# Performance work log

Hardware: AMD Instinct MI355X
Metric: run time of the kernel (lower is better)

The kernel has to match this reference:

```python
import jax, jax.numpy as jnp
import numpy as np

B, T, D, M = 32, 2048, 128, 256   # batch, seq_len, pitch vocab d, encoder_output_dim m
FILTERS = [256, 256, 256]
TAU = 1.0                          # gumbel_temperature
ALPHA_INV = 1.0 / (D * 100)        # W init value: 1/alpha, alpha = d*100


def causal_dilated_conv(x, w, b, dilation):
    """x: [B,T,Cin], w: [K,Cin,Cout], causal left padding."""
    k = w.shape[0]
    pad = (k - 1) * dilation
    y = jax.lax.conv_general_dilated(
        x, w, window_strides=(1,), padding=[(pad, 0)],
        rhs_dilation=(dilation,),
        dimension_numbers=('NWC', 'WIO', 'NWC'))
    return y + b


def slow_weight_model(batch, w0, b0, w1, b1, w2, b2, w_out, b_out):
    """DilatedConvBlock: stack of causal dilated convs (relu) + 1x1 readout to m logits."""
    h = jax.nn.relu(causal_dilated_conv(batch, w0, b0, dilation=1))
    h = jax.nn.relu(causal_dilated_conv(h, w1, b1, dilation=2))
    h = jax.nn.relu(causal_dilated_conv(h, w2, b2, dilation=4))
    return causal_dilated_conv(h, w_out, b_out, dilation=1)  # [B,T,M] logits


def setup_inputs() -> dict:
    key = jax.random.key(0)
    ks = jax.random.split(key, 9)
    def glorot(k, shape):
        fan_in = np.prod(shape[:-1])
        return (jax.random.normal(k, shape, jnp.float32) / np.sqrt(fan_in)).astype(jnp.float32)
    return {
        'batch': jax.random.uniform(ks[0], (B, T, D), jnp.float32),
        'w0': glorot(ks[1], (2, D, FILTERS[0])), 'b0': jnp.zeros((FILTERS[0],), jnp.float32),
        'w1': glorot(ks[2], (2, FILTERS[0], FILTERS[1])), 'b1': jnp.zeros((FILTERS[1],), jnp.float32),
        'w2': glorot(ks[3], (2, FILTERS[1], FILTERS[2])), 'b2': jnp.zeros((FILTERS[2],), jnp.float32),
        'w_out': glorot(ks[4], (1, FILTERS[2], M)), 'b_out': jnp.zeros((M,), jnp.float32),
    }


def reference(batch, w0, b0, w1, b1, w2, b2, w_out, b_out):
    logits = slow_weight_model(batch, w0, b0, w1, b1, w2, b2, w_out, b_out)  # [B,T,M]
    # short_term_method == 'softmax_normalize_after'
    h_src = jax.nn.softmax(logits / TAU, axis=2)  # [B,T,M]
    s_tar = batch                                  # [B,T,D]
    W0 = jnp.full((B, M, D), ALPHA_INV, jnp.float32)

    def step(W, hs):
        h, s = hs                                              # [B,M], [B,D]
        num = jnp.einsum('bm,bmd->bd', h, W)                   # readout
        prob = num / jnp.sum(num, axis=-1, keepdims=True)      # normalize-after
        W_new = W + h[:, :, None] * s[:, None, :]              # outer-product fast-weight update
        return W_new, prob

    W_final, probs = jax.lax.scan(
        step, W0, (jnp.swapaxes(h_src, 0, 1), jnp.swapaxes(s_tar, 0, 1)))
    probs = jnp.swapaxes(probs, 0, 1)  # [B,T,D]
    return probs, W_final
```

## Files before the change

### kernel.cpp

```cpp
#include <hip/hip_runtime.h>

using u16 = unsigned short;
using u32 = unsigned int;
using short8 = __attribute__((ext_vector_type(8))) short;
using short4v = __attribute__((ext_vector_type(4))) short;
using bf16x8 = __attribute__((ext_vector_type(8))) __bf16;
using f32x4 = __attribute__((ext_vector_type(4))) float;

#define ALPHA_INV (1.0f / (128.0f * 100.0f))

__device__ __forceinline__ u32 swz(u32 off, u32 row) { return off ^ ((row & 7u) << 4); }

__device__ __forceinline__ u16 f2bf(float x) {
  u32 u = __float_as_uint(x);
  u32 r = u + 0x7fffu + ((u >> 16) & 1u);
  return (u16)(r >> 16);
}

__device__ __forceinline__ float bf2f(u16 x) {
  u32 u = ((u32)x) << 16;
  return __uint_as_float(u);
}

__device__ __forceinline__ f32x4 mfma(bf16x8 a, bf16x8 b, f32x4 c) {
  return __builtin_amdgcn_mfma_f32_16x16x32_bf16(a, b, c, 0, 0, 0);
}

__device__ __forceinline__ void gl16(const void* g, void* l) {
  __builtin_amdgcn_global_load_lds(
      (const __attribute__((address_space(1))) unsigned int*)g,
      (__attribute__((address_space(3))) unsigned int*)l, 16, 0, 0);
}

__global__ __launch_bounds__(256) void prep(
    const float* __restrict__ batch,
    const float* __restrict__ w0, const float* __restrict__ w1,
    const float* __restrict__ w2, const float* __restrict__ wo,
    u16* __restrict__ o0, u16* __restrict__ o1,
    u16* __restrict__ o2, u16* __restrict__ o3,
    u16* __restrict__ ST) {
  __shared__ u16 L[64 * 129];
  int blk = blockIdx.x;
  if (blk < 1536) {
    const float* w; u16* o; int cin;
    if (blk < 256)       { w = w0; o = o0; cin = 128; }
    else if (blk < 768)  { w = w1; o = o1; cin = 256; blk -= 256; }
    else if (blk < 1280) { w = w2; o = o2; cin = 256; blk -= 768; }
    else                 { w = wo; o = o3; cin = 256; blk -= 1280; }
    int idx = blk * 256 + threadIdx.x;
    int row = idx >> 8, n = idx & 255;
    int tap = row / cin, c = row - tap * cin;
    int kc = c >> 6, ci = c & 63;
    u32 sb = (u32)(ci * 2) ^ ((u32)(n & 7) << 4);
    o[((size_t)tap * 256 + n) * cin + kc * 64 + (sb >> 1)] = f2bf(w[idx]);
    return;
  }
  blk -= 1536;
  const int tid = threadIdx.x;
  const int t0 = (blk & 31) * 64;
  const int b = blk >> 5;
  const float* src = batch + ((size_t)b * 2048 + t0) * 128;
#pragma unroll
  for (int it = 0; it < 4; ++it) {
    int s = tid + it * 256;
    int t = s >> 4, c8 = s & 15;
    float4 v0 = *(const float4*)(src + t * 128 + c8 * 8);
    float4 v1 = *(const float4*)(src + t * 128 + c8 * 8 + 4);
    u16* p = &L[t * 129 + c8 * 8];
    p[0] = f2bf(v0.x); p[1] = f2bf(v0.y); p[2] = f2bf(v0.z); p[3] = f2bf(v0.w);
    p[4] = f2bf(v1.x); p[5] = f2bf(v1.y); p[6] = f2bf(v1.z); p[7] = f2bf(v1.w);
  }
  __syncthreads();
  u16* dst = ST + (size_t)b * 128 * 2048 + t0;
#pragma unroll
  for (int it = 0; it < 4; ++it) {
    int s = tid + it * 256;
    int oct = s & 7, d = s >> 3;
    short8 v;
#pragma unroll
    for (int j = 0; j < 8; ++j) v[j] = (short)L[(oct * 8 + j) * 129 + d];
    *(short8*)(dst + (size_t)d * 2048 + oct * 8) = v;
  }
}

__global__ __launch_bounds__(512) void conv_first(
    const float* __restrict__ in, const u16* __restrict__ wt,
    const float* __restrict__ bias, u16* __restrict__ out) {
  constexpr int CIN = 128, BN = 256;
  __shared__ alignas(16) u16 Al[128 * 64];
  __shared__ alignas(16) u16 Bl[256 * 64];

  const int tid = threadIdx.x;
  const int wid = tid >> 6, lane = tid & 63;
  const int wr = wid >> 2, wc = wid & 3;
  const int lg = lane >> 4, lq = lane & 15;
  const int row0 = blockIdx.x * 128;
  const int tloc0 = row0 & 2047;

  f32x4 acc[4][4];
#pragma unroll
  for (int i = 0; i < 4; ++i)
#pragma unroll
    for (int j = 0; j < 4; ++j) acc[i][j] = (f32x4)0.0f;

#pragma unroll
  for (int tap = 0; tap < 2; ++tap) {
    const int shift = 1 - tap;
#pragma unroll
    for (int kc = 0; kc < 2; ++kc) {
#pragma unroll
      for (int it = 0; it < 2; ++it) {
        int gi = tid + it * 512;
        int r = gi >> 3, cg = gi & 7;
        short8 v = (short8)0;
        if (!(tloc0 == 0 && r < shift)) {
          const float* src = in + (size_t)(row0 + r - shift) * CIN + kc * 64 + cg * 8;
          float4 a = *(const float4*)src;
          float4 b2 = *(const float4*)(src + 4);
          v[0] = (short)f2bf(a.x);  v[1] = (short)f2bf(a.y);
          v[2] = (short)f2bf(a.z);  v[3] = (short)f2bf(a.w);
          v[4] = (short)f2bf(b2.x); v[5] = (short)f2bf(b2.y);
          v[6] = (short)f2bf(b2.z); v[7] = (short)f2bf(b2.w);
        }
        *(short8*)((char*)Al + swz(r * 128 + cg * 16, (u32)(r - shift + 8))) = v;
      }
      {
        const u16* wtb = wt + ((size_t)(tap * 256)) * CIN + kc * 64;
#pragma unroll
        for (int it = 0; it < 4; ++it) {
          int gi = tid + it * 512;
          int n = gi >> 3, cg = gi & 7;
          gl16(wtb + (size_t)n * CIN + cg * 8, (char*)Bl + it * 8192 + wid * 1024);
        }
      }
      __syncthreads();
#pragma unroll
      for (int ks = 0; ks < 2; ++ks) {
        bf16x8 af[4], bfr[4];
#pragma unroll
        for (int mi = 0; mi < 4; ++mi) {
          int r = wr * 64 + mi * 16 + lq;
          af[mi] = *(const bf16x8*)((const char*)Al +
                                    swz(r * 128 + ks * 64 + lg * 16, (u32)(r - shift + 8)));
        }
#pragma unroll
        for (int ni = 0; ni < 4; ++ni) {
          int n = wc * 64 + ni * 16 + lq;
          bfr[ni] = *(const bf16x8*)((const char*)Bl + swz(n * 128 + ks * 64 + lg * 16, n));
        }
#pragma unroll
        for (int mi = 0; mi < 4; ++mi)
#pragma unroll
          for (int ni = 0; ni < 4; ++ni)
            acc[mi][ni] = mfma(af[mi], bfr[ni], acc[mi][ni]);
      }
      __syncthreads();
    }
  }

  float bcol[4];
#pragma unroll
  for (int ni = 0; ni < 4; ++ni) bcol[ni] = bias[wc * 64 + ni * 16 + lq];
#pragma unroll
  for (int mi = 0; mi < 4; ++mi)
#pragma unroll
    for (int ni = 0; ni < 4; ++ni)
#pragma unroll
      for (int rr = 0; rr < 4; ++rr) {
        float v = fmaxf(acc[mi][ni][rr] + bcol[ni], 0.0f);
        int row = row0 + wr * 64 + mi * 16 + lg * 4 + rr;
        int col = wc * 64 + ni * 16 + lq;
        int ci = col & 63;
        u32 sb = (u32)(ci * 2) ^ ((u32)(row & 7) << 4);
        out[(size_t)row * BN + wc * 64 + (sb >> 1)] = f2bf(v);
      }
}

template <int DIL>
__global__ __launch_bounds__(512) void conv_mid(
    const u16* __restrict__ in, const u16* __restrict__ wt,
    const float* __restrict__ bias, u16* __restrict__ out) {
  constexpr int CIN = 256, BN = 256;
  __shared__ alignas(16) u16 Al[136 * 64];
  __shared__ alignas(16) u16 Bl[256 * 64];

  const int tid = threadIdx.x;
  const int wid = tid >> 6, lane = tid & 63;
  const int wr = wid >> 2, wc = wid & 3;
  const int lg = lane >> 4, lq = lane & 15;
  const int row0 = blockIdx.x * 128;
  const int tloc0 = row0 & 2047;

  f32x4 acc[4][4];
#pragma unroll
  for (int i = 0; i < 4; ++i)
#pragma unroll
    for (int j = 0; j < 4; ++j) acc[i][j] = (f32x4)0.0f;

#pragma unroll
  for (int kc = 0; kc < 4; ++kc) {
#pragma unroll
    for (int p = 0; p < 2; ++p) {
      int gi = tid + p * 512;
      int r = gi >> 3, cg = gi & 7;
      gl16(in + (size_t)(row0 - DIL + r) * CIN + kc * 64 + cg * 8,
           (char*)Al + p * 8192 + wid * 1024);
    }
    if (wid == 0)
      gl16(in + (size_t)(row0 - DIL + 128 + (lane >> 3)) * CIN + kc * 64 + (lane & 7) * 8,
           (char*)Al + 16384);
    {
      const u16* wtb = wt + (size_t)0 * 256 * CIN + kc * 64;
#pragma unroll
      for (int p = 0; p < 4; ++p) {
        int gi = tid + p * 512;
        int n = gi >> 3, cg = gi & 7;
        gl16(wtb + (size_t)n * CIN + cg * 8, (char*)Bl + p * 8192 + wid * 1024);
      }
    }
    __syncthreads();
    if (tloc0 == 0) {
      if (tid < DIL * 8) *(short8*)((char*)Al + tid * 16) = (short8)0;
      __syncthreads();
    }
#pragma unroll
    for (int ks = 0; ks < 2; ++ks) {
      bf16x8 af[4], bfr[4];
#pragma unroll
      for (int mi = 0; mi < 4; ++mi) {
        int r = wr * 64 + mi * 16 + lq;
        af[mi] = *(const bf16x8*)((const char*)Al +
                                  swz(r * 128 + ks * 64 + lg * 16, (u32)(r - DIL + 8)));
      }
#pragma unroll
      for (int ni = 0; ni < 4; ++ni) {
        int n = wc * 64 + ni * 16 + lq;
        bfr[ni] = *(const bf16x8*)((const char*)Bl + swz(n * 128 + ks * 64 + lg * 16, n));
      }
#pragma unroll
      for (int mi = 0; mi < 4; ++mi)
#pragma unroll
        for (int ni = 0; ni < 4; ++ni)
          acc[mi][ni] = mfma(af[mi], bfr[ni], acc[mi][ni]);
    }
    __syncthreads();
    {
      const u16* wtb = wt + (size_t)1 * 256 * CIN + kc * 64;
#pragma unroll
      for (int p = 0; p < 4; ++p) {
        int gi = tid + p * 512;
        int n = gi >> 3, cg = gi & 7;
        gl16(wtb + (size_t)n * CIN + cg * 8, (char*)Bl + p * 8192 + wid * 1024);
      }
    }
    __syncthreads();
#pragma unroll
    for (int ks = 0; ks < 2; ++ks) {
      bf16x8 af[4], bfr[4];
#pragma unroll
      for (int mi = 0; mi < 4; ++mi) {
        int r = wr * 64 + mi * 16 + lq;
        af[mi] = *(const bf16x8*)((const char*)Al +
                                  swz((r + DIL) * 128 + ks * 64 + lg * 16, (u32)(r + 8)));
      }
#pragma unroll
      for (int ni = 0; ni < 4; ++ni) {
        int n = wc * 64 + ni * 16 + lq;
        bfr[ni] = *(const bf16x8*)((const char*)Bl + swz(n * 128 + ks * 64 + lg * 16, n));
      }
#pragma unroll
      for (int mi = 0; mi < 4; ++mi)
#pragma unroll
        for (int ni = 0; ni < 4; ++ni)
          acc[mi][ni] = mfma(af[mi], bfr[ni], acc[mi][ni]);
    }
    __syncthreads();
  }

  float bcol[4];
#pragma unroll
  for (int ni = 0; ni < 4; ++ni) bcol[ni] = bias[wc * 64 + ni * 16 + lq];
#pragma unroll
  for (int mi = 0; mi < 4; ++mi)
#pragma unroll
    for (int ni = 0; ni < 4; ++ni)
#pragma unroll
      for (int rr = 0; rr < 4; ++rr) {
        float v = fmaxf(acc[mi][ni][rr] + bcol[ni], 0.0f);
        int row = row0 + wr * 64 + mi * 16 + lg * 4 + rr;
        int col = wc * 64 + ni * 16 + lq;
        int ci = col & 63;
        u32 sb = (u32)(ci * 2) ^ ((u32)(row & 7) << 4);
        out[(size_t)row * BN + wc * 64 + (sb >> 1)] = f2bf(v);
      }
}

__global__ __launch_bounds__(512) void conv_last(
    const u16* __restrict__ in, const u16* __restrict__ wt,
    const float* __restrict__ bias, u16* __restrict__ out) {
  constexpr int CIN = 256, BN = 256;
  __shared__ alignas(16) u16 Al[128 * 64];
  __shared__ alignas(16) u16 Bl[256 * 64];
  __shared__ float redA[4][128];
  __shared__ float redB[4][128];

  const int tid = threadIdx.x;
  const int wid = tid >> 6, lane = tid & 63;
  const int wr = wid >> 2, wc = wid & 3;
  const int lg = lane >> 4, lq = lane & 15;
  const int row0 = blockIdx.x * 128;

  f32x4 acc[4][4];
#pragma unroll
  for (int i = 0; i < 4; ++i)
#pragma unroll
    for (int j = 0; j < 4; ++j) acc[i][j] = (f32x4)0.0f;

#pragma unroll
  for (int kc = 0; kc < 4; ++kc) {
#pragma unroll
    for (int it = 0; it < 2; ++it) {
      int gi = tid + it * 512;
      int r = gi >> 3, cg = gi & 7;
      gl16(in + (size_t)(row0 + r) * CIN + kc * 64 + cg * 8,
           (char*)Al + it * 8192 + wid * 1024);
    }
    {
      const u16* wtb = wt + kc * 64;
#pragma unroll
      for (int it = 0; it < 4; ++it) {
        int gi = tid + it * 512;
        int n = gi >> 3, cg = gi & 7;
        gl16(wtb + (size_t)n * CIN + cg * 8, (char*)Bl + it * 8192 + wid * 1024);
      }
    }
    __syncthreads();
#pragma unroll
    for (int ks = 0; ks < 2; ++ks) {
      bf16x8 af[4], bfr[4];
#pragma unroll
      for (int mi = 0; mi < 4; ++mi) {
        int r = wr * 64 + mi * 16 + lq;
        af[mi] = *(const bf16x8*)((const char*)Al +
                                  swz(r * 128 + ks * 64 + lg * 16, (u32)(r + 8)));
      }
#pragma unroll
      for (int ni = 0; ni < 4; ++ni) {
        int n = wc * 64 + ni * 16 + lq;
        bfr[ni] = *(const bf16x8*)((const char*)Bl + swz(n * 128 + ks * 64 + lg * 16, n));
      }
#pragma unroll
      for (int mi = 0; mi < 4; ++mi)
#pragma unroll
        for (int ni = 0; ni < 4; ++ni)
          acc[mi][ni] = mfma(af[mi], bfr[ni], acc[mi][ni]);
    }
    __syncthreads();
  }

  float bcol[4];
#pragma unroll
  for (int ni = 0; ni < 4; ++ni) bcol[ni] = bias[wc * 64 + ni * 16 + lq];
#pragma unroll
  for (int mi = 0; mi < 4; ++mi)
#pragma unroll
    for (int ni = 0; ni < 4; ++ni)
#pragma unroll
      for (int rr = 0; rr < 4; ++rr) acc[mi][ni][rr] += bcol[ni];

  float tmx[4][4];
#pragma unroll
  for (int mi = 0; mi < 4; ++mi)
#pragma unroll
    for (int rr = 0; rr < 4; ++rr) {
      float v = fmaxf(fmaxf(acc[mi][0][rr], acc[mi][1][rr]),
                      fmaxf(acc[mi][2][rr], acc[mi][3][rr]));
#pragma unroll
      for (int off = 1; off < 16; off <<= 1) v = fmaxf(v, __shfl_xor(v, off));
      if (lq == 0) redA[wc][wr * 64 + mi * 16 + lg * 4 + rr] = v;
    }
  __syncthreads();
#pragma unroll
  for (int mi = 0; mi < 4; ++mi)
#pragma unroll
    for (int rr = 0; rr < 4; ++rr) {
      int rb = wr * 64 + mi * 16 + lg * 4 + rr;
      tmx[mi][rr] = fmaxf(fmaxf(redA[0][rb], redA[1][rb]),
                          fmaxf(redA[2][rb], redA[3][rb]));
    }
#pragma unroll
  for (int mi = 0; mi < 4; ++mi)
#pragma unroll
    for (int rr = 0; rr < 4; ++rr) {
      float s = 0.0f;
#pragma unroll
      for (int ni = 0; ni < 4; ++ni) {
        float p = __expf(acc[mi][ni][rr] - tmx[mi][rr]);
        acc[mi][ni][rr] = p;
        s += p;
      }
#pragma unroll
      for (int off = 1; off < 16; off <<= 1) s += __shfl_xor(s, off);
      if (lq == 0) redB[wc][wr * 64 + mi * 16 + lg * 4 + rr] = s;
    }
  __syncthreads();
#pragma unroll
  for (int mi = 0; mi < 4; ++mi)
#pragma unroll
    for (int rr = 0; rr < 4; ++rr) {
      int rb = wr * 64 + mi * 16 + lg * 4 + rr;
      float inv = 1.0f / (redB[0][rb] + redB[1][rb] + redB[2][rb] + redB[3][rb]);
      int row = row0 + rb;
#pragma unroll
      for (int ni = 0; ni < 4; ++ni) {
        int col = wc * 64 + ni * 16 + lq;
        out[(size_t)row * BN + col] = f2bf(acc[mi][ni][rr] * inv);
      }
    }
}

__global__ __launch_bounds__(512) void gchunk(
    const u16* __restrict__ H, const u16* __restrict__ ST,
    u16* __restrict__ G0, u16* __restrict__ G1) {
  constexpr int M = 256, T = 2048;
  __shared__ alignas(16) u16 Hl[128 * 128];
  __shared__ alignas(16) u16 Sl[128 * 128];
  const int tid = threadIdx.x;
  const int wid = tid >> 6, lane = tid & 63;
  const int dg = wid >> 2, mg = wid & 3;
  const int lg = lane >> 4, lq = lane & 15;
  const int b = blockIdx.x, mh = blockIdx.y, j = blockIdx.z;
  u16* G = (mh == 0 ? G0 : G1);

#pragma unroll
  for (int it = 0; it < 4; ++it) {
    int s = tid + it * 512;
    int t = s >> 4, c8 = s & 15;
    short8 v = *(const short8*)(H + ((size_t)b * T + j * 128 + t) * M + mh * 128 + c8 * 8);
#pragma unroll
    for (int jj = 0; jj < 8; ++jj) {
      int ml = c8 * 8 + jj;
      *(u16*)((char*)Hl + swz(ml * 256 + t * 2, ml)) = (u16)v[jj];
    }
  }
#pragma unroll
  for (int it = 0; it < 4; ++it) {
    int s = tid + it * 512;
    int d = s >> 4, c8 = s & 15;
    *(short8*)((char*)Sl + swz(d * 256 + c8 * 16, d)) =
        *(const short8*)(ST + ((size_t)b * 128 + d) * T + j * 128 + c8 * 8);
  }
  __syncthreads();

  f32x4 acc[4][2];
#pragma unroll
  for (int di = 0; di < 4; ++di)
#pragma unroll
    for (int mi = 0; mi < 2; ++mi) acc[di][mi] = (f32x4)0.0f;

#pragma unroll
  for (int ks = 0; ks < 4; ++ks) {
    bf16x8 sfrag[4];
#pragma unroll
    for (int di = 0; di < 4; ++di) {
      int d = dg * 64 + di * 16 + lq;
      sfrag[di] = *(const bf16x8*)((const char*)Sl + swz(d * 256 + ks * 64 + lg * 16, d));
    }
#pragma unroll
    for (int mi = 0; mi < 2; ++mi) {
      int ml = mg * 32 + mi * 16 + lq;
      bf16x8 hfrag =
          *(const bf16x8*)((const char*)Hl + swz(ml * 256 + ks * 64 + lg * 16, ml));
#pragma unroll
      for (int di = 0; di < 4; ++di) acc[di][mi] = mfma(sfrag[di], hfrag, acc[di][mi]);
    }
  }

  u16* Gj = G + (((size_t)b * 16 + j) << 14);
#pragma unroll
  for (int di = 0; di < 4; ++di)
#pragma unroll
    for (int mi = 0; mi < 2; ++mi)
#pragma unroll
      for (int rr = 0; rr < 4; ++rr) {
        int d = dg * 64 + di * 16 + lg * 4 + rr;
        int ml = mg * 32 + mi * 16 + lq;
        Gj[d * 128 + ml] = f2bf(acc[di][mi][rr]);
      }
}

__global__ __launch_bounds__(256) void prefix_wfin(
    u16* __restrict__ G0, u16* __restrict__ G1, float* __restrict__ wfin) {
  __shared__ float Wl[16][132];
  const int b = blockIdx.x, mh = blockIdx.y, ds = blockIdx.z;
  u16* G = mh ? G1 : G0;
  const int tid = threadIdx.x;
  const int mo = tid & 15, dg = tid >> 4;
  const int d = ds * 16 + dg;
  size_t base = (((size_t)b * 16) << 14) + d * 128 + mo * 8;
  float acc[8];
#pragma unroll
  for (int k = 0; k < 8; ++k) acc[k] = ALPHA_INV;
  for (int j = 0; j < 16; ++j) {
    u16* p = G + base + ((size_t)j << 14);
    short8 g = *(short8*)p;
    short8 c;
#pragma unroll
    for (int k = 0; k < 8; ++k) c[k] = (short)f2bf(acc[k]);
    *(short8*)p = c;
#pragma unroll
    for (int k = 0; k < 8; ++k) acc[k] += bf2f((u16)g[k]);
  }
#pragma unroll
  for (int k = 0; k < 8; ++k) Wl[dg][mo * 8 + k] = acc[k];
  __syncthreads();
  const int ml = tid >> 1, dq = tid & 1;
  const int dl0 = dq * 8;
  float* dst = wfin + ((size_t)b * 256 + mh * 128 + ml) * 128 + ds * 16 + dl0;
  float4 v0 = make_float4(Wl[dl0][ml], Wl[dl0 + 1][ml], Wl[dl0 + 2][ml], Wl[dl0 + 3][ml]);
  float4 v1 = make_float4(Wl[dl0 + 4][ml], Wl[dl0 + 5][ml], Wl[dl0 + 6][ml], Wl[dl0 + 7][ml]);
  *(float4*)dst = v0;
  *(float4*)(dst + 4) = v1;
}

__global__ __launch_bounds__(512) void attn_chunk(
    const u16* __restrict__ H, const u16* __restrict__ ST,
    const u16* __restrict__ C0, const u16* __restrict__ C1,
    float* __restrict__ out) {
  constexpr int M = 256, D = 128, T = 2048;
  __shared__ alignas(16) u16 Hi[128 * 256];
  __shared__ alignas(16) u16 Sl[128 * 128];
  __shared__ alignas(16) u16 Ct[128 * 128];

  const int tid = threadIdx.x;
  const int wid = tid >> 6, lane = tid & 63;
  const int lg = lane >> 4, lq = lane & 15;
  const int b = blockIdx.x, i = blockIdx.y;
  const size_t hrow0 = (size_t)b * T + i * 128;
  const size_t coff = ((size_t)b * 16 + i) * (128 * 128);

  bf16x8 aq[8];
  {
    const u16* qrow = H + (hrow0 + wid * 16 + lq) * M;
#pragma unroll
    for (int ks = 0; ks < 8; ++ks) aq[ks] = *(const bf16x8*)(qrow + ks * 32 + lg * 8);
  }

  short8 ct1r[4];
#pragma unroll
  for (int it = 0; it < 4; ++it) {
    int s = tid + it * 512;
    int d = s >> 4, c8 = s & 15;
    ct1r[it] = *(const short8*)(C1 + coff + d * 128 + c8 * 8);
  }

  {
    int r = wid * 16 + lq;
#pragma unroll
    for (int ks = 0; ks < 8; ++ks)
      *(short8*)((char*)Hi + swz(r * 512 + ks * 64 + lg * 16, r)) =
          __builtin_bit_cast(short8, aq[ks]);
  }
#pragma unroll
  for (int it = 0; it < 4; ++it) {
    int s = tid + it * 512;
    int d = s >> 4, c8 = s & 15;
    *(short8*)((char*)Sl + swz(d * 256 + c8 * 16, d)) =
        *(const short8*)(ST + ((size_t)b * D + d) * T + i * 128 + c8 * 8);
  }
#pragma unroll
  for (int it = 0; it < 4; ++it) {
    int s = tid + it * 512;
    int d = s >> 4, c8 = s & 15;
    *(short8*)((char*)Ct + swz(d * 256 + c8 * 16, d)) = *(const short8*)(C0 + coff + d * 128 + c8 * 8);
  }
  __syncthreads();

  f32x4 accO[8];
#pragma unroll
  for (int df = 0; df < 8; ++df) accO[df] = (f32x4)0.0f;
#pragma unroll
  for (int ks = 0; ks < 4; ++ks)
#pragma unroll
    for (int df = 0; df < 8; ++df) {
      int d = df * 16 + lq;
      bf16x8 bf = *(const bf16x8*)((const char*)Ct + swz(d * 256 + ks * 64 + lg * 16, d));
      accO[df] = mfma(aq[ks], bf, accO[df]);
    }
  f32x4 accP[8];
#pragma unroll
  for (int cf = 0; cf < 8; ++cf) accP[cf] = (f32x4)0.0f;
#pragma unroll
  for (int ks = 0; ks < 8; ++ks)
#pragma unroll
    for (int cf = 0; cf < 8; ++cf) {
      int tt = cf * 16 + lq;
      bf16x8 bf = *(const bf16x8*)((const char*)Hi + swz(tt * 512 + ks * 64 + lg * 16, tt));
      accP[cf] = mfma(aq[ks], bf, accP[cf]);
    }
  __syncthreads();

#pragma unroll
  for (int it = 0; it < 4; ++it) {
    int s = tid + it * 512;
    int d = s >> 4, c8 = s & 15;
    *(short8*)((char*)Ct + swz(d * 256 + c8 * 16, d)) = ct1r[it];
  }
  char* Pw = (char*)Hi + wid * 4096;
#pragma unroll
  for (int cf = 0; cf < 8; ++cf)
#pragma unroll
    for (int rr = 0; rr < 4; ++rr) {
      int ql = lg * 4 + rr;
      int tl = cf * 16 + lq;
      float v = accP[cf][rr];
      if (tl >= wid * 16 + ql) v = 0.0f;
      *(u16*)(Pw + swz(ql * 256 + tl * 2, ql)) = f2bf(v);
    }
  __syncthreads();

#pragma unroll
  for (int ks = 0; ks < 4; ++ks)
#pragma unroll
    for (int df = 0; df < 8; ++df) {
      int d = df * 16 + lq;
      bf16x8 bf = *(const bf16x8*)((const char*)Ct + swz(d * 256 + ks * 64 + lg * 16, d));
      accO[df] = mfma(aq[4 + ks], bf, accO[df]);
    }
#pragma unroll
  for (int ks = 0; ks < 4; ++ks) {
    bf16x8 a = *(const bf16x8*)(Pw + swz(lq * 256 + ks * 64 + lg * 16, lq));
#pragma unroll
    for (int df = 0; df < 8; ++df) {
      int d = df * 16 + lq;
      bf16x8 bf = *(const bf16x8*)((const char*)Sl + swz(d * 256 + ks * 64 + lg * 16, d));
      accO[df] = mfma(a, bf, accO[df]);
    }
  }

#pragma unroll
  for (int rr = 0; rr < 4; ++rr) {
    float ssum = 0.0f;
#pragma unroll
    for (int df = 0; df < 8; ++df) ssum += accO[df][rr];
#pragma unroll
    for (int off = 1; off < 16; off <<= 1) ssum += __shfl_xor(ssum, off);
    float inv = 1.0f / ssum;
    size_t row = hrow0 + wid * 16 + lg * 4 + rr;
#pragma unroll
    for (int df = 0; df < 8; ++df)
      out[row * D + df * 16 + lq] = accO[df][rr] * inv;
  }
}

extern "C" void kernel_launch(void* const* d_in, const int* in_sizes, int n_in,
                              void* d_out, int out_size, void* d_ws, size_t ws_size,
                              hipStream_t stream) {
  const float* batch = (const float*)d_in[0];
  const float* w0 = (const float*)d_in[1];
  const float* b0 = (const float*)d_in[2];
  const float* w1 = (const float*)d_in[3];
  const float* b1 = (const float*)d_in[4];
  const float* w2 = (const float*)d_in[5];
  const float* b2 = (const float*)d_in[6];
  const float* wo = (const float*)d_in[7];
  const float* bo = (const float*)d_in[8];

  const size_t SZ_S = 16777216;
  const size_t SZ_BUF = 33554432;
  const size_t ST_OFF = 88080384;
  const size_t NEED = ST_OFF + SZ_S;
  if (ws_size < NEED) return;

  char* ws = (char*)d_ws;
  u16* bufA = (u16*)(ws + SZ_S);
  u16* bufB = (u16*)(ws + SZ_S + SZ_BUF);
  u16* Wt0 = (u16*)(ws + SZ_S + 2 * SZ_BUF);
  u16* Wt1 = Wt0 + 2 * 256 * 128;
  u16* Wt2 = Wt1 + 2 * 256 * 256;
  u16* Wt3 = Wt2 + 2 * 256 * 256;
  u16* ST = (u16*)(ws + ST_OFF);
  u16* G0 = (u16*)ws;
  u16* G1 = (u16*)(ws + 2 * SZ_S);
  float* probs = (float*)d_out;
  float* wfin = probs + (size_t)32 * 2048 * 128;

  prep<<<2560, 256, 0, stream>>>(batch, w0, w1, w2, wo, Wt0, Wt1, Wt2, Wt3, ST);

  conv_first<<<512, 512, 0, stream>>>(batch, Wt0, b0, bufA);
  conv_mid<2><<<512, 512, 0, stream>>>(bufA, Wt1, b1, bufB);
  conv_mid<4><<<512, 512, 0, stream>>>(bufB, Wt2, b2, bufA);
  conv_last<<<512, 512, 0, stream>>>(bufA, Wt3, bo, bufB);

  gchunk<<<dim3(32, 2, 16), 512, 0, stream>>>(bufB, ST, G0, G1);
  prefix_wfin<<<dim3(32, 2, 8), 256, 0, stream>>>(G0, G1, wfin);
  attn_chunk<<<dim3(32, 16), 512, 0, stream>>>(bufB, ST, G0, G1, probs);
}
```

Baseline: 190.7 us.

## Double-buffer LDS tiles in conv_mid and conv_last to overlap loads with MFMA

Shared A/B tiles in the mid and last conv kernels become two buffers. The next K-chunk (and tap) is prefetched with asynchronous global-to-LDS loads while the current one is multiplied, and explicit vmcnt waits replace most __syncthreads. In conv_mid the two taps now run as eight flat iterations, and the input tile is reloaded for each tap. There is no barrier after compute before a buffer is overwritten, so a fast wave can start writing the next buffer while slower waves still read it.

New measurement: 172.7 us. -9.4%, faster.

```diff
diff --git a/kernel.cpp b/kernel.cpp
--- a/kernel.cpp
+++ b/kernel.cpp
@@ -181,8 +181,8 @@
     const u16* __restrict__ in, const u16* __restrict__ wt,
     const float* __restrict__ bias, u16* __restrict__ out) {
   constexpr int CIN = 256, BN = 256;
-  __shared__ alignas(16) u16 Al[136 * 64];
-  __shared__ alignas(16) u16 Bl[256 * 64];
+  __shared__ alignas(16) u16 Al[2][136 * 64];
+  __shared__ alignas(16) u16 Bl[2][256 * 64];
 
   const int tid = threadIdx.x;
   const int wid = tid >> 6, lane = tid & 63;
@@ -197,31 +197,46 @@
 #pragma unroll
     for (int j = 0; j < 4; ++j) acc[i][j] = (f32x4)0.0f;
 
-#pragma unroll
-  for (int kc = 0; kc < 4; ++kc) {
-#pragma unroll
-    for (int p = 0; p < 2; ++p) {
-      int gi = tid + p * 512;
-      int r = gi >> 3, cg = gi & 7;
-      gl16(in + (size_t)(row0 - DIL + r) * CIN + kc * 64 + cg * 8,
-           (char*)Al + p * 8192 + wid * 1024);
-    }
-    if (wid == 0)
-      gl16(in + (size_t)(row0 - DIL + 128 + (lane >> 3)) * CIN + kc * 64 + (lane & 7) * 8,
-           (char*)Al + 16384);
-    {
-      const u16* wtb = wt + (size_t)0 * 256 * CIN + kc * 64;
-#pragma unroll
-      for (int p = 0; p < 4; ++p) {
-        int gi = tid + p * 512;
-        int n = gi >> 3, cg = gi & 7;
-        gl16(wtb + (size_t)n * CIN + cg * 8, (char*)Bl + p * 8192 + wid * 1024);
-      }
-    }
-    __syncthreads();
-    if (tloc0 == 0) {
-      if (tid < DIL * 8) *(short8*)((char*)Al + tid * 16) = (short8)0;
-      __syncthreads();
+#define STAGE_MID(BUF, KC, TAP)                                                          \
+  {                                                                                      \
+    _Pragma("unroll") for (int p = 0; p < 2; ++p) {                                      \
+      int gi = tid + p * 512;                                                            \
+      gl16(in + (size_t)(row0 - DIL + (gi >> 3)) * CIN + (KC)*64 + (gi & 7) * 8,         \
+           (char*)Al[BUF] + p * 8192 + wid * 1024);                                      \
+    }                                                                                    \
+    if (wid == 0)                                                                        \
+      gl16(in + (size_t)(row0 - DIL + 128 + (lane >> 3)) * CIN + (KC)*64 + (lane & 7) * 8,\
+           (char*)Al[BUF] + 16384);                                                      \
+    const u16* wtb = wt + (size_t)(TAP)*256 * CIN + (KC)*64;                             \
+    _Pragma("unroll") for (int p = 0; p < 4; ++p) {                                      \
+      int gi = tid + p * 512;                                                            \
+      gl16(wtb + (size_t)(gi >> 3) * CIN + (gi & 7) * 8,                                 \
+           (char*)Bl[BUF] + p * 8192 + wid * 1024);                                      \
+    }                                                                                    \
+  }
+
+  STAGE_MID(0, 0, 0);
+
+#pragma unroll
+  for (int it8 = 0; it8 < 8; ++it8) {
+    const int buf = it8 & 1;
+    const int tap = it8 & 1;
+    const int kc = it8 >> 1;
+    if (it8 < 7) {
+      const int nkc = (it8 + 1) >> 1, ntap = (it8 + 1) & 1, nbuf = (it8 + 1) & 1;
+      STAGE_MID(nbuf, nkc, ntap);
+      if (wid == 0)
+        asm volatile("s_waitcnt vmcnt(7)" ::: "memory");
+      else
+        asm volatile("s_waitcnt vmcnt(6)" ::: "memory");
+    } else {
+      asm volatile("s_waitcnt vmcnt(0)" ::: "memory");
+    }
+    __builtin_amdgcn_s_barrier();
+    if (tap == 0 && tloc0 == 0) {
+      if (tid < DIL * 8) *(short8*)((char*)Al[buf] + tid * 16) = (short8)0;
+      asm volatile("s_waitcnt lgkmcnt(0)" ::: "memory");
+      __builtin_amdgcn_s_barrier();
     }
 #pragma unroll
     for (int ks = 0; ks < 2; ++ks) {
@@ -229,13 +244,17 @@
 #pragma unroll
       for (int mi = 0; mi < 4; ++mi) {
         int r = wr * 64 + mi * 16 + lq;
-        af[mi] = *(const bf16x8*)((const char*)Al +
-                                  swz(r * 128 + ks * 64 + lg * 16, (u32)(r - DIL + 8)));
+        if (tap == 0)
+          af[mi] = *(const bf16x8*)((const char*)Al[buf] +
+                                    swz(r * 128 + ks * 64 + lg * 16, (u32)(r - DIL + 8)));
+        else
+          af[mi] = *(const bf16x8*)((const char*)Al[buf] +
+                                    swz((r + DIL) * 128 + ks * 64 + lg * 16, (u32)(r + 8)));
       }
 #pragma unroll
       for (int ni = 0; ni < 4; ++ni) {
         int n = wc * 64 + ni * 16 + lq;
-        bfr[ni] = *(const bf16x8*)((const char*)Bl + swz(n * 128 + ks * 64 + lg * 16, n));
+        bfr[ni] = *(const bf16x8*)((const char*)Bl[buf] + swz(n * 128 + ks * 64 + lg * 16, n));
       }
 #pragma unroll
       for (int mi = 0; mi < 4; ++mi)
@@ -243,39 +262,8 @@
         for (int ni = 0; ni < 4; ++ni)
           acc[mi][ni] = mfma(af[mi], bfr[ni], acc[mi][ni]);
     }
-    __syncthreads();
-    {
-      const u16* wtb = wt + (size_t)1 * 256 * CIN + kc * 64;
-#pragma unroll
-      for (int p = 0; p < 4; ++p) {
-        int gi = tid + p * 512;
-        int n = gi >> 3, cg = gi & 7;
-        gl16(wtb + (size_t)n * CIN + cg * 8, (char*)Bl + p * 8192 + wid * 1024);
-      }
-    }
-    __syncthreads();
-#pragma unroll
-    for (int ks = 0; ks < 2; ++ks) {
-      bf16x8 af[4], bfr[4];
-#pragma unroll
-      for (int mi = 0; mi < 4; ++mi) {
-        int r = wr * 64 + mi * 16 + lq;
-        af[mi] = *(const bf16x8*)((const char*)Al +
-                                  swz((r + DIL) * 128 + ks * 64 + lg * 16, (u32)(r + 8)));
-      }
-#pragma unroll
-      for (int ni = 0; ni < 4; ++ni) {
-        int n = wc * 64 + ni * 16 + lq;
-        bfr[ni] = *(const bf16x8*)((const char*)Bl + swz(n * 128 + ks * 64 + lg * 16, n));
-      }
-#pragma unroll
-      for (int mi = 0; mi < 4; ++mi)
-#pragma unroll
-        for (int ni = 0; ni < 4; ++ni)
-          acc[mi][ni] = mfma(af[mi], bfr[ni], acc[mi][ni]);
-    }
-    __syncthreads();
-  }
+  }
+#undef STAGE_MID
 
   float bcol[4];
 #pragma unroll
@@ -299,8 +287,8 @@
     const u16* __restrict__ in, const u16* __restrict__ wt,
     const float* __restrict__ bias, u16* __restrict__ out) {
   constexpr int CIN = 256, BN = 256;
-  __shared__ alignas(16) u16 Al[128 * 64];
-  __shared__ alignas(16) u16 Bl[256 * 64];
+  __shared__ alignas(16) u16 Al[2][128 * 64];
+  __shared__ alignas(16) u16 Bl[2][256 * 64];
   __shared__ float redA[4][128];
   __shared__ float redB[4][128];
 
@@ -316,38 +304,46 @@
 #pragma unroll
     for (int j = 0; j < 4; ++j) acc[i][j] = (f32x4)0.0f;
 
-#pragma unroll
-  for (int kc = 0; kc < 4; ++kc) {
-#pragma unroll
-    for (int it = 0; it < 2; ++it) {
-      int gi = tid + it * 512;
-      int r = gi >> 3, cg = gi & 7;
-      gl16(in + (size_t)(row0 + r) * CIN + kc * 64 + cg * 8,
-           (char*)Al + it * 8192 + wid * 1024);
-    }
-    {
-      const u16* wtb = wt + kc * 64;
-#pragma unroll
-      for (int it = 0; it < 4; ++it) {
-        int gi = tid + it * 512;
-        int n = gi >> 3, cg = gi & 7;
-        gl16(wtb + (size_t)n * CIN + cg * 8, (char*)Bl + it * 8192 + wid * 1024);
-      }
-    }
-    __syncthreads();
+#define STAGE_LAST(BUF, KC)                                                              \
+  {                                                                                      \
+    _Pragma("unroll") for (int p = 0; p < 2; ++p) {                                      \
+      int gi = tid + p * 512;                                                            \
+      gl16(in + (size_t)(row0 + (gi >> 3)) * CIN + (KC)*64 + (gi & 7) * 8,               \
+           (char*)Al[BUF] + p * 8192 + wid * 1024);                                      \
+    }                                                                                    \
+    const u16* wtb = wt + (KC)*64;                                                       \
+    _Pragma("unroll") for (int p = 0; p < 4; ++p) {                                      \
+      int gi = tid + p * 512;                                                            \
+      gl16(wtb + (size_t)(gi >> 3) * CIN + (gi & 7) * 8,                                 \
+           (char*)Bl[BUF] + p * 8192 + wid * 1024);                                      \
+    }                                                                                    \
+  }
+
+  STAGE_LAST(0, 0);
+
+#pragma unroll
+  for (int it4 = 0; it4 < 4; ++it4) {
+    const int buf = it4 & 1;
+    if (it4 < 3) {
+      STAGE_LAST((it4 + 1) & 1, it4 + 1);
+      asm volatile("s_waitcnt vmcnt(6)" ::: "memory");
+    } else {
+      asm volatile("s_waitcnt vmcnt(0)" ::: "memory");
+    }
+    __builtin_amdgcn_s_barrier();
 #pragma unroll
     for (int ks = 0; ks < 2; ++ks) {
       bf16x8 af[4], bfr[4];
 #pragma unroll
       for (int mi = 0; mi < 4; ++mi) {
         int r = wr * 64 + mi * 16 + lq;
-        af[mi] = *(const bf16x8*)((const char*)Al +
+        af[mi] = *(const bf16x8*)((const char*)Al[buf] +
                                   swz(r * 128 + ks * 64 + lg * 16, (u32)(r + 8)));
       }
 #pragma unroll
       for (int ni = 0; ni < 4; ++ni) {
         int n = wc * 64 + ni * 16 + lq;
-        bfr[ni] = *(const bf16x8*)((const char*)Bl + swz(n * 128 + ks * 64 + lg * 16, n));
+        bfr[ni] = *(const bf16x8*)((const char*)Bl[buf] + swz(n * 128 + ks * 64 + lg * 16, n));
       }
 #pragma unroll
       for (int mi = 0; mi < 4; ++mi)
@@ -355,8 +351,9 @@
         for (int ni = 0; ni < 4; ++ni)
           acc[mi][ni] = mfma(af[mi], bfr[ni], acc[mi][ni]);
     }
-    __syncthreads();
-  }
+  }
+#undef STAGE_LAST
+  __syncthreads();
 
   float bcol[4];
 #pragma unroll
```
